# Performance work log

Hardware: AMD Instinct MI355X
Metric: run time of the kernel (lower is better)

The kernel has to match this reference:

```python
import jax, jax.numpy as jnp
import numpy as np

E, H, L = 512, 1024, 4
VS, VT = 32000, 32000
B, SS, TT = 64, 48, 48
PAD = 0


def _cell(x, h, c, Wih, Whh, bih, bhh):
    # torch.nn.LSTMCell math: gate order i, f, g, o
    g = x @ Wih.T + h @ Whh.T + bih + bhh
    i, f, gg, o = jnp.split(g, 4, axis=-1)
    c = jax.nn.sigmoid(f) * c + jax.nn.sigmoid(i) * jnp.tanh(gg)
    h = jax.nn.sigmoid(o) * jnp.tanh(c)
    return h, c


def setup_inputs() -> dict:
    key = jax.random.key(0)
    ks = jax.random.split(key, 14)
    s = 0.05
    d = {}
    d['src_tokens'] = jax.random.randint(ks[0], (SS, B), 0, VS, dtype=jnp.int32)
    d['tgt_tokens'] = jax.random.randint(ks[1], (TT, B), 0, VT, dtype=jnp.int32)
    d['src_emb'] = jax.random.normal(ks[2], (VS, E)) * s
    d['tgt_emb'] = jax.random.normal(ks[3], (VT, E)) * s
    d['enc_Wih0'] = jax.random.normal(ks[4], (4 * H, E)) * s
    d['enc_WihR'] = jax.random.normal(ks[5], (L - 1, 4 * H, H)) * s
    d['enc_Whh'] = jax.random.normal(ks[6], (L, 4 * H, H)) * s
    d['enc_bih'] = jnp.zeros((L, 4 * H))
    d['enc_bhh'] = jnp.zeros((L, 4 * H))
    d['dec_Wih0'] = jax.random.normal(ks[7], (4 * H, E + H)) * s
    d['dec_WihR'] = jax.random.normal(ks[8], (L - 1, 4 * H, H)) * s
    d['dec_Whh'] = jax.random.normal(ks[9], (L, 4 * H, H)) * s
    d['dec_bih'] = jnp.zeros((L, 4 * H))
    d['dec_bhh'] = jnp.zeros((L, 4 * H))
    d['att_vec_W'] = jax.random.normal(ks[10], (H, 2 * H)) * s
    d['readout_W'] = jax.random.normal(ks[11], (VT, H)) * s
    return d


def _forward(src_tokens, tgt_tokens, src_emb, tgt_emb, enc_Wih0, enc_WihR,
             enc_Whh, enc_bih, enc_bhh, dec_Wih0, dec_WihR, dec_Whh, dec_bih,
             dec_bhh, att_vec_W, readout_W):
    src_x = src_emb[src_tokens]                      # [SS, B, E]
    h0 = jnp.zeros((L, B, H), src_emb.dtype)
    c0 = jnp.zeros((L, B, H), src_emb.dtype)

    def enc_step(carry, x_t):
        h, c = carry
        inp = x_t
        hs, cs = [], []
        for l in range(L):
            Wih = enc_Wih0 if l == 0 else enc_WihR[l - 1]
            hn, cn = _cell(inp, h[l], c[l], Wih, enc_Whh[l], enc_bih[l], enc_bhh[l])
            hs.append(hn); cs.append(cn)
            inp = hn
        return (jnp.stack(hs), jnp.stack(cs)), inp

    (hT, cT), enc_out = jax.lax.scan(enc_step, (h0, c0), src_x)
    src_enc = enc_out.transpose(1, 0, 2)             # [B, SS, H]

    # decoder init: last encoder layer (h, c) copied to every decoder layer
    hd = jnp.tile(hT[-1][None], (L, 1, 1))
    cd = jnp.tile(cT[-1][None], (L, 1, 1))
    tgt_x = tgt_emb[tgt_tokens[:-1]]                 # [TT-1, B, E]
    att0 = jnp.zeros((B, H), src_emb.dtype)

    def dec_step(carry, y_t):
        h, c, att = carry
        inp = jnp.concatenate([y_t, att], axis=-1)   # input feeding
        hs, cs = [], []
        for l in range(L):
            Wih = dec_Wih0 if l == 0 else dec_WihR[l - 1]
            hn, cn = _cell(inp, h[l], c[l], Wih, dec_Whh[l], dec_bih[l], dec_bhh[l])
            hs.append(hn); cs.append(cn)
            inp = hn
        h_top = hs[-1]
        # global attention, 'dot' score (full-length seqs -> all-zero mask is a no-op)
        scores = jnp.einsum('bsh,bh->bs', src_enc, h_top)
        alpha = jax.nn.softmax(scores, axis=-1)
        ctx = jnp.einsum('bs,bsh->bh', alpha, src_enc)
        att_t = jnp.tanh(jnp.concatenate([h_top, ctx], axis=-1) @ att_vec_W.T)
        return (jnp.stack(hs), jnp.stack(cs), att_t), att_t

    _, att_ves = jax.lax.scan(dec_step, (hd, cd, att0), tgt_x)  # [TT-1, B, H]

    logp = jax.nn.log_softmax(att_ves @ readout_W.T, axis=-1)   # [TT-1, B, VT]
    gold = tgt_tokens[1:]
    gold_lp = jnp.take_along_axis(logp, gold[..., None], axis=-1)[..., 0]
    mask = (gold != PAD).astype(logp.dtype)
    return (gold_lp * mask).sum(axis=0)              # [B]


def reference(src_tokens, tgt_tokens, src_emb, tgt_emb, enc_Wih0, enc_WihR,
              enc_Whh, enc_bih, enc_bhh, dec_Wih0, dec_WihR, dec_Whh, dec_bih,
              dec_bhh, att_vec_W, readout_W):
    return _forward(src_tokens, tgt_tokens, src_emb, tgt_emb, enc_Wih0,
                    enc_WihR, enc_Whh, enc_bih, enc_bhh, dec_Wih0, dec_WihR,
                    dec_Whh, dec_bih, dec_bhh, att_vec_W, readout_W)
```

## Files before the change

### kernel.cpp

```cpp
#include <hip/hip_runtime.h>


typedef __attribute__((ext_vector_type(8))) short bf16x8;
typedef __attribute__((ext_vector_type(4))) float f32x4;

#define SMEM_BYTES 32768
#define SMEM_RO    49152

#define NMT_SYNC_LIGHT()                                   \
  do {                                                     \
    asm volatile("s_waitcnt lgkmcnt(0)" ::: "memory");     \
    __builtin_amdgcn_s_barrier();                          \
    __builtin_amdgcn_sched_barrier(0);                     \
  } while (0)

__device__ __forceinline__ float bf2f(ushort u) {
  union { uint i; float f; } v; v.i = ((uint)u) << 16; return v.f;
}
__device__ __forceinline__ ushort f2bf(float x) {
  union { float f; uint i; } v; v.f = x;
  uint r = (v.i + 0x7fffu + ((v.i >> 16) & 1u)) >> 16;
  return (ushort)r;
}
__device__ __forceinline__ float sigm(float x) {
  return __fdividef(1.f, 1.f + __expf(-x));
}
__device__ __forceinline__ float tanhf_fast(float x) {
  const float e = __expf(2.f * x);
  return 1.f - __fdividef(2.f, e + 1.f);
}

__device__ __forceinline__ void gemm_term(
    const ushort* __restrict__ A, int lda,
    const ushort* __restrict__ W, int ldw,
    int K, int m0, int n0,
    f32x4 acc[4], char* s)
{
  char* sA0 = s;
  char* sB0 = s + 8192;
  char* sA1 = s + 16384;
  char* sB1 = s + 24576;
  const int tid = threadIdx.x;
  const int lane = tid & 63;
  const int w = tid >> 6;
  const int r0 = tid >> 3;
  const int cge = (tid & 7) << 3;
  const ushort* Arow0 = A + (size_t)(m0 + r0) * lda + cge;
  const ushort* Arow1 = A + (size_t)(m0 + r0 + 32) * lda + cge;
  const ushort* Wrow0 = W + (size_t)(n0 + r0) * ldw + cge;
  const ushort* Wrow1 = W + (size_t)(n0 + r0 + 32) * ldw + cge;
  const int so0 = r0 * 128 + (((tid & 7) << 4) ^ ((r0 & 7) << 4));
  const int so1 = so0 + 4096;

  uint4 a0 = *reinterpret_cast<const uint4*>(Arow0);
  uint4 a1 = *reinterpret_cast<const uint4*>(Arow1);
  uint4 b0 = *reinterpret_cast<const uint4*>(Wrow0);
  uint4 b1 = *reinterpret_cast<const uint4*>(Wrow1);
  *reinterpret_cast<uint4*>(sA0 + so0) = a0;
  *reinterpret_cast<uint4*>(sA0 + so1) = a1;
  *reinterpret_cast<uint4*>(sB0 + so0) = b0;
  *reinterpret_cast<uint4*>(sB0 + so1) = b1;
  if (K > 64) {
    a0 = *reinterpret_cast<const uint4*>(Arow0 + 64);
    a1 = *reinterpret_cast<const uint4*>(Arow1 + 64);
    b0 = *reinterpret_cast<const uint4*>(Wrow0 + 64);
    b1 = *reinterpret_cast<const uint4*>(Wrow1 + 64);
  }
  const int axor = (lane & 7) << 4;
  const int arow = (w * 16 + (lane & 15)) * 128;
  const int brow = (lane & 15) * 128;
  const int kb0 = (lane >> 4) << 4;
  for (int kt = 0; kt < K; kt += 64) {
    char* cA = (kt & 64) ? sA1 : sA0;
    char* cB = (kt & 64) ? sB1 : sB0;
    char* nA = (kt & 64) ? sA0 : sA1;
    char* nB = (kt & 64) ? sB0 : sB1;
    __syncthreads();
    if (kt + 64 < K) {
      *reinterpret_cast<uint4*>(nA + so0) = a0;
      *reinterpret_cast<uint4*>(nA + so1) = a1;
      *reinterpret_cast<uint4*>(nB + so0) = b0;
      *reinterpret_cast<uint4*>(nB + so1) = b1;
      if (kt + 128 < K) {
        a0 = *reinterpret_cast<const uint4*>(Arow0 + kt + 128);
        a1 = *reinterpret_cast<const uint4*>(Arow1 + kt + 128);
        b0 = *reinterpret_cast<const uint4*>(Wrow0 + kt + 128);
        b1 = *reinterpret_cast<const uint4*>(Wrow1 + kt + 128);
      }
    }
#pragma unroll
    for (int ks = 0; ks < 2; ++ks) {
      const int kb = ks * 64 + kb0;
      bf16x8 af = *reinterpret_cast<const bf16x8*>(cA + arow + (kb ^ axor));
#pragma unroll
      for (int nf = 0; nf < 4; ++nf) {
        bf16x8 bfr = *reinterpret_cast<const bf16x8*>(
            cB + nf * 2048 + brow + (kb ^ axor));
        acc[nf] = __builtin_amdgcn_mfma_f32_16x16x32_bf16(af, bfr, acc[nf], 0, 0, 0);
      }
    }
  }
  __syncthreads();
}

__device__ __forceinline__ void store_f32(
    float* __restrict__ out, int ldo, int m0, int n0, f32x4 acc[4])
{
  const int tid = threadIdx.x, lane = tid & 63, w = tid >> 6;
  const int rbase = w * 16 + ((lane >> 4) << 2);
  const int cb = lane & 15;
#pragma unroll
  for (int nf = 0; nf < 4; ++nf)
#pragma unroll
    for (int r = 0; r < 4; ++r)
      out[(size_t)(m0 + rbase + r) * ldo + n0 + nf * 16 + cb] = acc[nf][r];
}

__device__ __forceinline__ void cell_store(
    float* smemF, f32x4 acc[4],
    float* __restrict__ c, ushort* __restrict__ hout,
    ushort* __restrict__ senc_t, int j0)
{
  const int tid = threadIdx.x, lane = tid & 63, w = tid >> 6;
  const int rbase = w * 16 + ((lane >> 4) << 2);
  const int cb = lane & 15;
  __syncthreads();
#pragma unroll
  for (int nf = 0; nf < 4; ++nf)
#pragma unroll
    for (int r = 0; r < 4; ++r)
      smemF[(rbase + r) * 68 + nf * 16 + cb] = acc[nf][r];
  __syncthreads();
#pragma unroll
  for (int i = 0; i < 4; ++i) {
    const int id = tid + i * 256;
    const int b = id >> 4, u = id & 15;
    const float g0 = smemF[b * 68 + u * 4 + 0];
    const float g1 = smemF[b * 68 + u * 4 + 1];
    const float g2 = smemF[b * 68 + u * 4 + 2];
    const float g3 = smemF[b * 68 + u * 4 + 3];
    const int off = b * 1024 + j0 + u;
    const float cold = c[off];
    const float cn = sigm(g1) * cold + sigm(g0) * tanhf_fast(g2);
    const float hv = sigm(g3) * tanhf_fast(cn);
    c[off] = cn;
    const ushort hb = f2bf(hv);
    hout[off] = hb;
    if (senc_t) senc_t[(size_t)b * 49152 + j0 + u] = hb;
  }
}

__global__ __launch_bounds__(256) void nmt_init(float* c, ushort* henc, ushort* attbf)
{
  const int idx = blockIdx.x * 256 + threadIdx.x;
  if (idx < 262144) c[idx] = 0.f;
  if (idx < 65536) {
    attbf[idx] = 0;
    henc[idx] = 0;
    henc[(size_t)1 * 49 * 65536 + idx] = 0;
    henc[(size_t)2 * 49 * 65536 + idx] = 0;
    henc[(size_t)3 * 49 * 65536 + idx] = 0;
  }
}

__global__ __launch_bounds__(256) void nmt_convperm(
    const float* __restrict__ in, ushort* __restrict__ out,
    int L, int Kin, int col0, int Kout)
{
  const size_t idx = (size_t)blockIdx.x * 256 + threadIdx.x;
  const size_t total = (size_t)L * 4096 * Kout;
  if (idx >= total) return;
  const int k = (int)(idx % Kout);
  const size_t rem = idx / Kout;
  const int rp = (int)(rem % 4096);
  const int l = (int)(rem / 4096);
  const int j = rp >> 2, g = rp & 3;
  out[idx] = f2bf(in[((size_t)l * 4096 + g * 1024 + j) * Kin + col0 + k]);
}

__global__ __launch_bounds__(256) void nmt_convplain(
    const float* __restrict__ in, ushort* __restrict__ out, size_t n)
{
  const size_t idx = (size_t)blockIdx.x * 256 + threadIdx.x;
  if (idx < n) out[idx] = f2bf(in[idx]);
}

__global__ __launch_bounds__(256) void nmt_bias(
    const float* __restrict__ bih, const float* __restrict__ bhh, float* __restrict__ bc)
{
  const int idx = blockIdx.x * 256 + threadIdx.x;
  if (idx >= 4 * 4096) return;
  const int rp = idx & 4095, l = idx >> 12;
  const int j = rp >> 2, g = rp & 3;
  bc[idx] = bih[l * 4096 + g * 1024 + j] + bhh[l * 4096 + g * 1024 + j];
}

__global__ __launch_bounds__(256) void nmt_gather(
    const int* __restrict__ tok, const float* __restrict__ emb,
    ushort* __restrict__ out, int rows)
{
  const size_t idx = (size_t)blockIdx.x * 256 + threadIdx.x;
  if (idx >= (size_t)rows * 512) return;
  const int k = (int)(idx & 511);
  const int r = (int)(idx >> 9);
  out[idx] = f2bf(emb[(size_t)tok[r] * 512 + k]);
}

__global__ __launch_bounds__(256) void nmt_pre(
    const ushort* __restrict__ A, const ushort* __restrict__ Wp,
    const float* __restrict__ bc0, float* __restrict__ out, int K)
{
  __shared__ __align__(16) char smem[SMEM_BYTES];
  const int m0 = blockIdx.x * 64, n0 = blockIdx.y * 64;
  const int lane = threadIdx.x & 63;
  const int cb = lane & 15;
  f32x4 acc[4];
#pragma unroll
  for (int nf = 0; nf < 4; ++nf) {
    const float bv = bc0[n0 + nf * 16 + cb];
#pragma unroll
    for (int r = 0; r < 4; ++r) acc[nf][r] = bv;
  }
  gemm_term(A, K, Wp, K, K, m0, n0, acc, smem);
  store_f32(out, 4096, m0, n0, acc);
}

__global__ __launch_bounds__(256) void nmt_decinit(
    const ushort* __restrict__ henc, float* c, ushort* h)
{
  const int idx = blockIdx.x * 256 + threadIdx.x;
  if (idx >= 65536) return;
  const ushort hv = henc[((size_t)3 * 49 + 48) * 65536 + idx];
  const float cv = c[3 * 65536 + idx];
  c[idx] = cv; c[65536 + idx] = cv; c[2 * 65536 + idx] = cv;
  h[idx] = hv; h[65536 + idx] = hv; h[2 * 65536 + idx] = hv; h[3 * 65536 + idx] = hv;
}

__global__ __launch_bounds__(256) void nmt_sv(
    const ushort* __restrict__ senc, const ushort* __restrict__ attW,
    ushort* __restrict__ SV)
{
  __shared__ __align__(16) char smem[SMEM_BYTES];
  const int b = blockIdx.x;
  const int n0 = blockIdx.y * 64;
  const int tid = threadIdx.x, lane = tid & 63, w = tid >> 6;
  const int rbase = w * 16 + ((lane >> 4) << 2), cb = lane & 15;
  f32x4 acc[4];
#pragma unroll
  for (int nf = 0; nf < 4; ++nf)
#pragma unroll
    for (int r = 0; r < 4; ++r) acc[nf][r] = 0.f;
  gemm_term(senc + (size_t)b * 49152, 1024, attW + 1024, 2048, 1024, 0, n0,
            acc, smem);
#pragma unroll
  for (int nf = 0; nf < 4; ++nf)
#pragma unroll
    for (int r = 0; r < 4; ++r) {
      const int row = rbase + r;
      if (row < 48)
        SV[(size_t)b * 49152 + row * 1024 + n0 + nf * 16 + cb] = f2bf(acc[nf][r]);
    }
}

__global__ __launch_bounds__(256) void nmt_enc_cell(
    int u, int lo, ushort* __restrict__ henc, ushort* __restrict__ srcenc,
    float* __restrict__ c,
    const ushort* __restrict__ WihR, const ushort* __restrict__ Whh,
    const float* __restrict__ X0, const float* __restrict__ bcE)
{
  __shared__ __align__(16) char smem[SMEM_BYTES];
  const int l = lo + blockIdx.y;
  const int t = u - l;
  const int n0 = blockIdx.x * 64;
  const int tid = threadIdx.x, lane = tid & 63, w = tid >> 6;
  const int rbase = w * 16 + ((lane >> 4) << 2), cb = lane & 15;
  f32x4 acc[4];
  if (l == 0) {
#pragma unroll
    for (int nf = 0; nf < 4; ++nf)
#pragma unroll
      for (int r = 0; r < 4; ++r)
        acc[nf][r] = X0[(size_t)t * 262144 + (size_t)(rbase + r) * 4096 + n0 + nf * 16 + cb];
  } else {
#pragma unroll
    for (int nf = 0; nf < 4; ++nf) {
      const float bv = bcE[l * 4096 + n0 + nf * 16 + cb];
#pragma unroll
      for (int r = 0; r < 4; ++r) acc[nf][r] = bv;
    }
    gemm_term(henc + ((size_t)(l - 1) * 49 + t + 1) * 65536, 1024,
              WihR + (size_t)(l - 1) * 4194304, 1024, 1024, 0, n0, acc, smem);
  }
  gemm_term(henc + ((size_t)l * 49 + t) * 65536, 1024,
            Whh + (size_t)l * 4194304, 1024, 1024, 0, n0, acc, smem);
  cell_store((float*)smem, acc, c + l * 65536,
             henc + ((size_t)l * 49 + t + 1) * 65536,
             (l == 3) ? (srcenc + t * 1024) : (ushort*)nullptr, n0 >> 2);
}

__global__ __launch_bounds__(256) void nmt_dec_stage(
    int l, const ushort* __restrict__ hp, ushort* __restrict__ hn,
    float* __restrict__ c,
    const ushort* __restrict__ Whh, const ushort* __restrict__ WihR,
    const ushort* __restrict__ Wd0a, const ushort* __restrict__ attbf,
    const float* __restrict__ Y0t, const float* __restrict__ bcD,
    float* __restrict__ pbuf)
{
  __shared__ __align__(16) char smem[SMEM_BYTES];
  const int n0 = blockIdx.x * 64;
  const int tid = threadIdx.x, lane = tid & 63, w = tid >> 6;
  const int rbase = w * 16 + ((lane >> 4) << 2), cb = lane & 15;
  f32x4 acc[4];
  if (blockIdx.y == 0) {
    if (l == 0) {
#pragma unroll
      for (int nf = 0; nf < 4; ++nf)
#pragma unroll
        for (int r = 0; r < 4; ++r) {
          const size_t o = (size_t)(rbase + r) * 4096 + n0 + nf * 16 + cb;
          acc[nf][r] = Y0t[o] + pbuf[o];
        }
      gemm_term(attbf, 1024, Wd0a, 1024, 1024, 0, n0, acc, smem);
    } else {
#pragma unroll
      for (int nf = 0; nf < 4; ++nf)
#pragma unroll
        for (int r = 0; r < 4; ++r)
          acc[nf][r] = pbuf[(size_t)l * 262144 + (size_t)(rbase + r) * 4096 + n0 + nf * 16 + cb];
      gemm_term(hn + (l - 1) * 65536, 1024, WihR + (size_t)(l - 1) * 4194304,
                1024, 1024, 0, n0, acc, smem);
    }
    cell_store((float*)smem, acc, c + l * 65536, hn + l * 65536,
               (ushort*)nullptr, n0 >> 2);
  } else {
    const int lp = (l + 1) & 3;
    if (lp == 0) {
#pragma unroll
      for (int nf = 0; nf < 4; ++nf)
#pragma unroll
        for (int r = 0; r < 4; ++r) acc[nf][r] = 0.f;
      gemm_term(hn, 1024, Whh, 1024, 1024, 0, n0, acc, smem);
    } else {
#pragma unroll
      for (int nf = 0; nf < 4; ++nf) {
        const float bv = bcD[lp * 4096 + n0 + nf * 16 + cb];
#pragma unroll
        for (int r = 0; r < 4; ++r) acc[nf][r] = bv;
      }
      gemm_term(hp + lp * 65536, 1024, Whh + (size_t)lp * 4194304,
                1024, 1024, 0, n0, acc, smem);
    }
    store_f32(pbuf + (size_t)lp * 262144, 4096, 0, n0, acc);
  }
}

__global__ __launch_bounds__(256) void nmt_partial0(
    const ushort* __restrict__ h0, const ushort* __restrict__ Whh0,
    float* __restrict__ pbuf)
{
  __shared__ __align__(16) char smem[SMEM_BYTES];
  const int n0 = blockIdx.x * 64;
  f32x4 acc[4];
#pragma unroll
  for (int nf = 0; nf < 4; ++nf)
#pragma unroll
    for (int r = 0; r < 4; ++r) acc[nf][r] = 0.f;
  gemm_term(h0, 1024, Whh0, 1024, 1024, 0, n0, acc, smem);
  store_f32(pbuf, 4096, 0, n0, acc);
}

__global__ __launch_bounds__(256) void nmt_attnAB(
    const ushort* __restrict__ h3, const ushort* __restrict__ senc,
    const ushort* __restrict__ SV, const ushort* __restrict__ attW,
    float* __restrict__ ctx2, float* __restrict__ hb)
{
  __shared__ __align__(16) char smem[SMEM_BYTES];
  const int bid = blockIdx.x;
  const int tid = threadIdx.x, lane = tid & 63, w = tid >> 6;
  if (bid < 64) {
    float* sc = (float*)smem;
    float* al = (float*)smem + 64;
    const int b = bid;
    const ushort* sb = senc + (size_t)b * 49152;
    const ushort* vb = SV + (size_t)b * 49152;
    float hreg[16];
#pragma unroll
    for (int q = 0; q < 16; ++q) hreg[q] = bf2f(h3[b * 1024 + lane * 16 + q]);
    for (int s = w; s < 48; s += 4) {
      const ushort* vr = sb + s * 1024 + lane * 16;
      float p = 0.f;
#pragma unroll
      for (int q = 0; q < 16; ++q) p += bf2f(vr[q]) * hreg[q];
      for (int d = 1; d < 64; d <<= 1) p += __shfl_xor(p, d);
      if (lane == 0) sc[s] = p;
    }
    __syncthreads();
    if (tid < 64) {
      const float v = (lane < 48) ? sc[lane] : -3.4e38f;
      float m = v;
      for (int d = 1; d < 64; d <<= 1) m = fmaxf(m, __shfl_xor(m, d));
      float e = (lane < 48) ? expf(v - m) : 0.f;
      float s = e;
      for (int d = 1; d < 64; d <<= 1) s += __shfl_xor(s, d);
      al[lane] = e / s;
    }
    __syncthreads();
    const int k0 = tid * 4;
    float a0 = 0, a1 = 0, a2 = 0, a3 = 0;
    for (int s = 0; s < 48; ++s) {
      const float als = al[s];
      const ushort* vr = vb + s * 1024 + k0;
      a0 += als * bf2f(vr[0]); a1 += als * bf2f(vr[1]);
      a2 += als * bf2f(vr[2]); a3 += als * bf2f(vr[3]);
    }
    ctx2[b * 1024 + k0 + 0] = a0; ctx2[b * 1024 + k0 + 1] = a1;
    ctx2[b * 1024 + k0 + 2] = a2; ctx2[b * 1024 + k0 + 3] = a3;
  } else {
    const int n0 = (bid - 64) * 64;
    f32x4 acc[4];
#pragma unroll
    for (int nf = 0; nf < 4; ++nf)
#pragma unroll
      for (int r = 0; r < 4; ++r) acc[nf][r] = 0.f;
    gemm_term(h3, 1024, attW, 2048, 1024, 0, n0, acc, smem);
    store_f32(hb, 1024, 0, n0, acc);
  }
}

__global__ __launch_bounds__(256) void nmt_attnSB(
    const float* __restrict__ ctx2, const float* __restrict__ hb,
    ushort* __restrict__ attbf, ushort* __restrict__ av_t)
{
  const int base = blockIdx.x * 1024 + threadIdx.x * 4;
#pragma unroll
  for (int k = 0; k < 4; ++k) {
    const int i = base + k;
    const ushort us = f2bf(tanhf_fast(hb[i] + ctx2[i]));
    attbf[i] = us;
    av_t[i] = us;
  }
}

__global__ __launch_bounds__(256) void nmt_readout(
    const ushort* __restrict__ attves, const ushort* __restrict__ routW,
    const int* __restrict__ tgt, float* __restrict__ pmax,
    float* __restrict__ psum, float* __restrict__ goldl)
{
  __shared__ __align__(16) char smem[SMEM_RO];
  const int g = blockIdx.x;
  const int n0 = blockIdx.y * 64;
  const int tid = threadIdx.x, lane = tid & 63, w = tid >> 6;
  const int rbase = w * 16 + ((lane >> 4) << 2), cb = lane & 15;
  const int r0 = tid >> 3;
  const int cge = (tid & 7) << 3;
  const int soX = r0 * 128 + (((tid & 7) << 4) ^ ((r0 & 7) << 4));
  const int axor = (lane & 7) << 4;
  const int arow = (w * 16 + (lane & 15)) * 128;
  const int brow = (lane & 15) * 128;
  const int kb0 = (lane >> 4) << 4;

  const ushort* A0r0 = attves + (size_t)(g * 128 + r0) * 1024 + cge;
  const ushort* A0r1 = attves + (size_t)(g * 128 + r0 + 32) * 1024 + cge;
  const ushort* A1r0 = attves + (size_t)(g * 128 + 64 + r0) * 1024 + cge;
  const ushort* A1r1 = attves + (size_t)(g * 128 + 64 + r0 + 32) * 1024 + cge;
  const ushort* Br0  = routW + (size_t)(n0 + r0) * 1024 + cge;
  const ushort* Br1  = routW + (size_t)(n0 + r0 + 32) * 1024 + cge;

  f32x4 acc[2][4];
#pragma unroll
  for (int mi = 0; mi < 2; ++mi)
#pragma unroll
    for (int nf = 0; nf < 4; ++nf)
#pragma unroll
      for (int r = 0; r < 4; ++r) acc[mi][nf][r] = 0.f;

  uint4 ra0 = *(const uint4*)(A0r0);
  uint4 ra1 = *(const uint4*)(A0r1);
  uint4 ra2 = *(const uint4*)(A1r0);
  uint4 ra3 = *(const uint4*)(A1r1);
  uint4 rb0 = *(const uint4*)(Br0);
  uint4 rb1 = *(const uint4*)(Br1);
  {
    char* sl = smem;
    *(uint4*)(sl + soX) = ra0;          *(uint4*)(sl + 4096 + soX) = ra1;
    *(uint4*)(sl + 8192 + soX) = ra2;   *(uint4*)(sl + 12288 + soX) = ra3;
    *(uint4*)(sl + 16384 + soX) = rb0;  *(uint4*)(sl + 20480 + soX) = rb1;
  }
  ra0 = *(const uint4*)(A0r0 + 64);
  ra1 = *(const uint4*)(A0r1 + 64);
  ra2 = *(const uint4*)(A1r0 + 64);
  ra3 = *(const uint4*)(A1r1 + 64);
  rb0 = *(const uint4*)(Br0 + 64);
  rb1 = *(const uint4*)(Br1 + 64);

  for (int kt = 0; kt < 1024; kt += 64) {
    NMT_SYNC_LIGHT();
    if (kt + 64 < 1024) {
      char* sl = smem + ((((kt >> 6) + 1) & 1) ? 24576 : 0);
      *(uint4*)(sl + soX) = ra0;          *(uint4*)(sl + 4096 + soX) = ra1;
      *(uint4*)(sl + 8192 + soX) = ra2;   *(uint4*)(sl + 12288 + soX) = ra3;
      *(uint4*)(sl + 16384 + soX) = rb0;  *(uint4*)(sl + 20480 + soX) = rb1;
      if (kt + 128 < 1024) {
        ra0 = *(const uint4*)(A0r0 + kt + 128);
        ra1 = *(const uint4*)(A0r1 + kt + 128);
        ra2 = *(const uint4*)(A1r0 + kt + 128);
        ra3 = *(const uint4*)(A1r1 + kt + 128);
        rb0 = *(const uint4*)(Br0 + kt + 128);
        rb1 = *(const uint4*)(Br1 + kt + 128);
      }
    }
    char* cur = smem + (((kt >> 6) & 1) ? 24576 : 0);
#pragma unroll
    for (int ks = 0; ks < 2; ++ks) {
      const int kb = (ks << 6) + kb0;
      bf16x8 bf0 = *(const bf16x8*)(cur + 16384 + 0 * 2048 + brow + (kb ^ axor));
      bf16x8 bf1 = *(const bf16x8*)(cur + 16384 + 1 * 2048 + brow + (kb ^ axor));
      bf16x8 bf2 = *(const bf16x8*)(cur + 16384 + 2 * 2048 + brow + (kb ^ axor));
      bf16x8 bf3 = *(const bf16x8*)(cur + 16384 + 3 * 2048 + brow + (kb ^ axor));
      bf16x8 af0 = *(const bf16x8*)(cur + arow + (kb ^ axor));
      bf16x8 af1 = *(const bf16x8*)(cur + 8192 + arow + (kb ^ axor));
      acc[0][0] = __builtin_amdgcn_mfma_f32_16x16x32_bf16(af0, bf0, acc[0][0], 0, 0, 0);
      acc[0][1] = __builtin_amdgcn_mfma_f32_16x16x32_bf16(af0, bf1, acc[0][1], 0, 0, 0);
      acc[0][2] = __builtin_amdgcn_mfma_f32_16x16x32_bf16(af0, bf2, acc[0][2], 0, 0, 0);
      acc[0][3] = __builtin_amdgcn_mfma_f32_16x16x32_bf16(af0, bf3, acc[0][3], 0, 0, 0);
      acc[1][0] = __builtin_amdgcn_mfma_f32_16x16x32_bf16(af1, bf0, acc[1][0], 0, 0, 0);
      acc[1][1] = __builtin_amdgcn_mfma_f32_16x16x32_bf16(af1, bf1, acc[1][1], 0, 0, 0);
      acc[1][2] = __builtin_amdgcn_mfma_f32_16x16x32_bf16(af1, bf2, acc[1][2], 0, 0, 0);
      acc[1][3] = __builtin_amdgcn_mfma_f32_16x16x32_bf16(af1, bf3, acc[1][3], 0, 0, 0);
    }
  }

#pragma unroll
  for (int mi = 0; mi < 2; ++mi) {
    const int gm = g * 2 + mi;
    if (gm >= 47) continue;
#pragma unroll
    for (int r = 0; r < 4; ++r) {
      float lm = fmaxf(fmaxf(acc[mi][0][r], acc[mi][1][r]),
                       fmaxf(acc[mi][2][r], acc[mi][3][r]));
      for (int d = 1; d < 16; d <<= 1) lm = fmaxf(lm, __shfl_xor(lm, d));
      float ls = 0.f;
#pragma unroll
      for (int nf = 0; nf < 4; ++nf) ls += expf(acc[mi][nf][r] - lm);
      for (int d = 1; d < 16; d <<= 1) ls += __shfl_xor(ls, d);
      const int grow = gm * 64 + rbase + r;
      if (cb == 0) {
        pmax[(size_t)grow * 500 + blockIdx.y] = lm;
        psum[(size_t)grow * 500 + blockIdx.y] = ls;
      }
      const int t = grow >> 6, b = grow & 63;
      const int gold = tgt[(t + 1) * 64 + b];
#pragma unroll
      for (int nf = 0; nf < 4; ++nf)
        if (n0 + nf * 16 + cb == gold) goldl[grow] = acc[mi][nf][r];
    }
  }
}

__global__ __launch_bounds__(64) void nmt_combine(
    const float* __restrict__ pmax, const float* __restrict__ psum,
    const float* __restrict__ goldl, const int* __restrict__ tgt,
    float* __restrict__ lpm)
{
  const int row = blockIdx.x;
  const int lane = threadIdx.x;
  float m = -3.4e38f, s = 0.f;
  for (int i = lane; i < 500; i += 64) {
    const float pm = pmax[(size_t)row * 500 + i];
    const float ps = psum[(size_t)row * 500 + i];
    if (pm > m) { s = s * expf(m - pm) + ps; m = pm; }
    else        { s += ps * expf(pm - m); }
  }
  for (int d = 1; d < 64; d <<= 1) {
    const float om = __shfl_xor(m, d), os = __shfl_xor(s, d);
    if (om > m) { s = s * expf(m - om) + os; m = om; }
    else        { s += os * expf(om - m); }
  }
  if (lane == 0) {
    const int t = row >> 6, b = row & 63;
    const int gold = tgt[(t + 1) * 64 + b];
    const float lp = goldl[row] - m - logf(s);
    lpm[row] = (gold != 0) ? lp : 0.f;
  }
}

__global__ __launch_bounds__(64) void nmt_final(
    const float* __restrict__ lpm, float* __restrict__ out)
{
  const int b = threadIdx.x;
  float s = 0.f;
  for (int t = 0; t < 47; ++t) s += lpm[t * 64 + b];
  out[b] = s;
}

extern "C" void kernel_launch(void* const* d_in, const int* in_sizes, int n_in,
                              void* d_out, int out_size, void* d_ws, size_t ws_size,
                              hipStream_t stream)
{
  (void)in_sizes; (void)n_in; (void)out_size; (void)ws_size;
  const int*   src_tok  = (const int*)d_in[0];
  const int*   tgt_tok  = (const int*)d_in[1];
  const float* src_emb  = (const float*)d_in[2];
  const float* tgt_emb  = (const float*)d_in[3];
  const float* eWih0    = (const float*)d_in[4];
  const float* eWihR    = (const float*)d_in[5];
  const float* eWhh     = (const float*)d_in[6];
  const float* ebih     = (const float*)d_in[7];
  const float* ebhh     = (const float*)d_in[8];
  const float* dWih0    = (const float*)d_in[9];
  const float* dWihR    = (const float*)d_in[10];
  const float* dWhh     = (const float*)d_in[11];
  const float* dbih     = (const float*)d_in[12];
  const float* dbhh     = (const float*)d_in[13];
  const float* attW_f   = (const float*)d_in[14];
  const float* routW_f  = (const float*)d_in[15];

  char* p = (char*)d_ws;
  auto alloc = [&](size_t bytes) { void* r = (void*)p; p += (bytes + 255) & ~(size_t)255; return r; };
  ushort* eWih0p = (ushort*)alloc((size_t)4096 * 512 * 2);
  ushort* eWihRp = (ushort*)alloc((size_t)3 * 4096 * 1024 * 2);
  ushort* eWhhp  = (ushort*)alloc((size_t)4 * 4096 * 1024 * 2);
  ushort* dWih0y = (ushort*)alloc((size_t)4096 * 512 * 2);
  ushort* dWih0a = (ushort*)alloc((size_t)4096 * 1024 * 2);
  ushort* dWihRp = (ushort*)alloc((size_t)3 * 4096 * 1024 * 2);
  ushort* dWhhp  = (ushort*)alloc((size_t)4 * 4096 * 1024 * 2);
  ushort* attWb  = (ushort*)alloc((size_t)1024 * 2048 * 2);
  ushort* routWb = (ushort*)alloc((size_t)32000 * 1024 * 2);
  ushort* srcx   = (ushort*)alloc((size_t)3072 * 512 * 2);
  ushort* tgtx   = (ushort*)alloc((size_t)3008 * 512 * 2);
  ushort* henc   = (ushort*)alloc((size_t)4 * 49 * 65536 * 2);
  ushort* hA     = (ushort*)alloc((size_t)4 * 65536 * 2);
  ushort* hB     = (ushort*)alloc((size_t)4 * 65536 * 2);
  ushort* srcenc = (ushort*)alloc((size_t)64 * 49152 * 2);
  ushort* SVbuf  = (ushort*)alloc((size_t)64 * 49152 * 2);
  ushort* attbf  = (ushort*)alloc((size_t)65536 * 2);
  ushort* attves = (ushort*)alloc((size_t)3072 * 1024 * 2);
  float*  ctx2   = (float*)alloc((size_t)65536 * 4);
  float*  hbuf   = (float*)alloc((size_t)65536 * 4);
  float*  pbuf   = (float*)alloc((size_t)4 * 262144 * 4);
  float*  X0     = (float*)alloc((size_t)3072 * 4096 * 4);
  float*  Y0     = (float*)alloc((size_t)3008 * 4096 * 4);
  float*  bcE    = (float*)alloc((size_t)16384 * 4);
  float*  bcD    = (float*)alloc((size_t)16384 * 4);
  float*  cbuf   = (float*)alloc((size_t)4 * 65536 * 4);
  float*  pmaxb  = (float*)alloc((size_t)3008 * 500 * 4);
  float*  psumb  = (float*)alloc((size_t)3008 * 500 * 4);
  float*  goldl  = (float*)alloc((size_t)3008 * 4);
  float*  lpm    = (float*)alloc((size_t)3008 * 4);

  const dim3 B256(256);
  auto g1 = [](size_t n) { return dim3((unsigned)((n + 255) / 256)); };

  nmt_init<<<g1(262144), B256, 0, stream>>>(cbuf, henc, attbf);

  nmt_convperm<<<g1((size_t)4096 * 512), B256, 0, stream>>>(eWih0, eWih0p, 1, 512, 0, 512);
  nmt_convperm<<<g1((size_t)3 * 4096 * 1024), B256, 0, stream>>>(eWihR, eWihRp, 3, 1024, 0, 1024);
  nmt_convperm<<<g1((size_t)4 * 4096 * 1024), B256, 0, stream>>>(eWhh, eWhhp, 4, 1024, 0, 1024);
  nmt_convperm<<<g1((size_t)4096 * 512), B256, 0, stream>>>(dWih0, dWih0y, 1, 1536, 0, 512);
  nmt_convperm<<<g1((size_t)4096 * 1024), B256, 0, stream>>>(dWih0, dWih0a, 1, 1536, 512, 1024);
  nmt_convperm<<<g1((size_t)3 * 4096 * 1024), B256, 0, stream>>>(dWihR, dWihRp, 3, 1024, 0, 1024);
  nmt_convperm<<<g1((size_t)4 * 4096 * 1024), B256, 0, stream>>>(dWhh, dWhhp, 4, 1024, 0, 1024);
  nmt_convplain<<<g1((size_t)1024 * 2048), B256, 0, stream>>>(attW_f, attWb, (size_t)1024 * 2048);
  nmt_convplain<<<g1((size_t)32000 * 1024), B256, 0, stream>>>(routW_f, routWb, (size_t)32000 * 1024);
  nmt_bias<<<g1(16384), B256, 0, stream>>>(ebih, ebhh, bcE);
  nmt_bias<<<g1(16384), B256, 0, stream>>>(dbih, dbhh, bcD);
  nmt_gather<<<g1((size_t)3072 * 512), B256, 0, stream>>>(src_tok, src_emb, srcx, 3072);
  nmt_gather<<<g1((size_t)3008 * 512), B256, 0, stream>>>(tgt_tok, tgt_emb, tgtx, 3008);

  nmt_pre<<<dim3(48, 64), B256, 0, stream>>>(srcx, eWih0p, bcE, X0, 512);
  nmt_pre<<<dim3(47, 64), B256, 0, stream>>>(tgtx, dWih0y, bcD, Y0, 512);

  for (int u = 0; u < 51; ++u) {
    const int lo = (u > 47) ? (u - 47) : 0;
    const int hi = (u < 3) ? u : 3;
    nmt_enc_cell<<<dim3(64, hi - lo + 1), B256, 0, stream>>>(
        u, lo, henc, srcenc, cbuf, eWihRp, eWhhp, X0, bcE);
  }
  nmt_decinit<<<g1(65536), B256, 0, stream>>>(henc, cbuf, hA);
  nmt_sv<<<dim3(64, 16), B256, 0, stream>>>(srcenc, attWb, SVbuf);
  nmt_partial0<<<dim3(64), B256, 0, stream>>>(hA, dWhhp, pbuf);

  for (int t = 0; t < 47; ++t) {
    ushort* hp = (t & 1) ? hB : hA;
    ushort* hn = (t & 1) ? hA : hB;
    for (int l = 0; l < 4; ++l) {
      nmt_dec_stage<<<dim3(64, 2), B256, 0, stream>>>(
          l, hp, hn, cbuf, dWhhp, dWihRp, dWih0a, attbf,
          Y0 + (size_t)t * 262144, bcD, pbuf);
    }
    nmt_attnAB<<<dim3(80), B256, 0, stream>>>(hn + 3 * 65536, srcenc, SVbuf,
                                              attWb, ctx2, hbuf);
    nmt_attnSB<<<dim3(64), B256, 0, stream>>>(ctx2, hbuf, attbf,
                                              attves + (size_t)t * 65536);
  }

  nmt_readout<<<dim3(24, 500), B256, 0, stream>>>(attves, routWb, tgt_tok,
                                                  pmaxb, psumb, goldl);
  nmt_combine<<<dim3(3008), dim3(64), 0, stream>>>(pmaxb, psumb, goldl, tgt_tok, lpm);
  nmt_final<<<dim3(1), dim3(64), 0, stream>>>(lpm, (float*)d_out);
}
```

Baseline: 4.191 ms.

## Fuse attention tanh/bf16 pack into decoder layer-0 GEMM load and batch attves

Removes the per-step nmt_attnSB kernel by having the decoder layer-0 stage compute tanh(hb+ctx) on the fly while staging the A operand into shared memory. hb and ctx are kept per step in large fp32 buffers, and all attention vectors are converted to bf16 for the readout in one batched kernel after the loop. This saves 47 kernel launches and their serial dependency gaps. In exchange, the layer-0 GEMM reads fp32 operands and uses 64KB of shared memory, which may reduce occupancy, and the tanh is recomputed by each of the 64 column blocks.

```diff
diff --git a/kernel.cpp b/kernel.cpp
--- a/kernel.cpp
+++ b/kernel.cpp
@@ -5,6 +5,7 @@
 typedef __attribute__((ext_vector_type(4))) float f32x4;
 
 #define SMEM_BYTES 32768
+#define SMEM_A     65536
 #define SMEM_RO    49152
 
 #define NMT_SYNC_LIGHT()                                   \
@@ -21,6 +22,9 @@
   union { float f; uint i; } v; v.f = x;
   uint r = (v.i + 0x7fffu + ((v.i >> 16) & 1u)) >> 16;
   return (ushort)r;
+}
+__device__ __forceinline__ uint pack2(float x, float y) {
+  return (uint)f2bf(x) | ((uint)f2bf(y) << 16);
 }
 __device__ __forceinline__ float sigm(float x) {
   return __fdividef(1.f, 1.f + __expf(-x));
@@ -103,6 +107,119 @@
   __syncthreads();
 }
 
+__device__ __forceinline__ void att_loadf(
+    const float* H0, const float* H1, const float* C0, const float* C1,
+    int kt, float4* fh, float4* fc)
+{
+#pragma unroll
+  for (int q = 0; q < 8; ++q) {
+    const int rh = q >> 2, sub = (q >> 1) & 1, vq = q & 1;
+    const float* hp_ = rh ? H1 : H0;
+    const float* cp_ = rh ? C1 : C0;
+    fh[q] = *reinterpret_cast<const float4*>(hp_ + kt + sub * 64 + vq * 4);
+    fc[q] = *reinterpret_cast<const float4*>(cp_ + kt + sub * 64 + vq * 4);
+  }
+}
+
+__device__ __forceinline__ void att_store(
+    char* buf, int soX, const float4* fh, const float4* fc)
+{
+#pragma unroll
+  for (int rh = 0; rh < 2; ++rh)
+#pragma unroll
+    for (int sub = 0; sub < 2; ++sub) {
+      const int q0 = rh * 4 + sub * 2;
+      const float4 u = fh[q0], v = fc[q0];
+      const float4 u2 = fh[q0 + 1], v2 = fc[q0 + 1];
+      uint4 o;
+      o.x = pack2(tanhf_fast(u.x + v.x), tanhf_fast(u.y + v.y));
+      o.y = pack2(tanhf_fast(u.z + v.z), tanhf_fast(u.w + v.w));
+      o.z = pack2(tanhf_fast(u2.x + v2.x), tanhf_fast(u2.y + v2.y));
+      o.w = pack2(tanhf_fast(u2.z + v2.z), tanhf_fast(u2.w + v2.w));
+      *reinterpret_cast<uint4*>(buf + sub * 8192 + rh * 4096 + soX) = o;
+    }
+}
+
+__device__ __forceinline__ void gemm_att(
+    const float* __restrict__ H, const float* __restrict__ C2,
+    const ushort* __restrict__ W, int ldw, int n0,
+    f32x4 acc[4], char* s)
+{
+  char* sA0 = s;
+  char* sB0 = s + 16384;
+  char* sA1 = s + 32768;
+  char* sB1 = s + 49152;
+  const int tid = threadIdx.x;
+  const int lane = tid & 63;
+  const int w = tid >> 6;
+  const int r0 = tid >> 3;
+  const int cge = (tid & 7) << 3;
+  const int soX = r0 * 128 + (((tid & 7) << 4) ^ ((r0 & 7) << 4));
+  const ushort* Wr0 = W + (size_t)(n0 + r0) * ldw + cge;
+  const ushort* Wr1 = W + (size_t)(n0 + r0 + 32) * ldw + cge;
+  const float* H0 = H + r0 * 1024 + cge;
+  const float* H1 = H + (r0 + 32) * 1024 + cge;
+  const float* C0 = C2 + r0 * 1024 + cge;
+  const float* C1 = C2 + (r0 + 32) * 1024 + cge;
+
+  float4 fh[8], fc[8];
+  uint4 b0, b1, b2, b3;
+  att_loadf(H0, H1, C0, C1, 0, fh, fc);
+  att_store(sA0, soX, fh, fc);
+  b0 = *reinterpret_cast<const uint4*>(Wr0);
+  b1 = *reinterpret_cast<const uint4*>(Wr1);
+  b2 = *reinterpret_cast<const uint4*>(Wr0 + 64);
+  b3 = *reinterpret_cast<const uint4*>(Wr1 + 64);
+  *reinterpret_cast<uint4*>(sB0 + soX) = b0;
+  *reinterpret_cast<uint4*>(sB0 + 4096 + soX) = b1;
+  *reinterpret_cast<uint4*>(sB0 + 8192 + soX) = b2;
+  *reinterpret_cast<uint4*>(sB0 + 12288 + soX) = b3;
+  att_loadf(H0, H1, C0, C1, 128, fh, fc);
+  b0 = *reinterpret_cast<const uint4*>(Wr0 + 128);
+  b1 = *reinterpret_cast<const uint4*>(Wr1 + 128);
+  b2 = *reinterpret_cast<const uint4*>(Wr0 + 192);
+  b3 = *reinterpret_cast<const uint4*>(Wr1 + 192);
+
+  const int axor = (lane & 7) << 4;
+  const int arow = (w * 16 + (lane & 15)) * 128;
+  const int brow = (lane & 15) * 128;
+  const int kb0 = (lane >> 4) << 4;
+  for (int kt = 0; kt < 1024; kt += 128) {
+    char* cA = (kt & 128) ? sA1 : sA0;
+    char* cB = (kt & 128) ? sB1 : sB0;
+    char* nA = (kt & 128) ? sA0 : sA1;
+    char* nB = (kt & 128) ? sB0 : sB1;
+    NMT_SYNC_LIGHT();
+    if (kt + 128 < 1024) {
+      att_store(nA, soX, fh, fc);
+      *reinterpret_cast<uint4*>(nB + soX) = b0;
+      *reinterpret_cast<uint4*>(nB + 4096 + soX) = b1;
+      *reinterpret_cast<uint4*>(nB + 8192 + soX) = b2;
+      *reinterpret_cast<uint4*>(nB + 12288 + soX) = b3;
+      if (kt + 256 < 1024) {
+        att_loadf(H0, H1, C0, C1, kt + 256, fh, fc);
+        b0 = *reinterpret_cast<const uint4*>(Wr0 + kt + 256);
+        b1 = *reinterpret_cast<const uint4*>(Wr1 + kt + 256);
+        b2 = *reinterpret_cast<const uint4*>(Wr0 + kt + 320);
+        b3 = *reinterpret_cast<const uint4*>(Wr1 + kt + 320);
+      }
+    }
+#pragma unroll
+    for (int ks = 0; ks < 4; ++ks) {
+      const int sb = (ks >> 1) * 8192;
+      const int kb = ((ks & 1) << 6) + kb0;
+      bf16x8 af = *reinterpret_cast<const bf16x8*>(cA + sb + arow + (kb ^ axor));
+#pragma unroll
+      for (int nf = 0; nf < 4; ++nf) {
+        bf16x8 bfr = *reinterpret_cast<const bf16x8*>(
+            cB + sb + nf * 2048 + brow + (kb ^ axor));
+        acc[nf] = __builtin_amdgcn_mfma_f32_16x16x32_bf16(af, bfr, acc[nf], 0, 0, 0);
+      }
+    }
+  }
+  __syncthreads();
+}
+
 __device__ __forceinline__ void store_f32(
     float* __restrict__ out, int ldo, int m0, int n0, f32x4 acc[4])
 {
@@ -150,12 +267,14 @@
   }
 }
 
-__global__ __launch_bounds__(256) void nmt_init(float* c, ushort* henc, ushort* attbf)
+__global__ __launch_bounds__(256) void nmt_init(
+    float* c, ushort* henc, float* hbAll, float* ctxAll)
 {
   const int idx = blockIdx.x * 256 + threadIdx.x;
   if (idx < 262144) c[idx] = 0.f;
   if (idx < 65536) {
-    attbf[idx] = 0;
+    hbAll[idx] = 0.f;
+    ctxAll[idx] = 0.f;
     henc[idx] = 0;
     henc[(size_t)1 * 49 * 65536 + idx] = 0;
     henc[(size_t)2 * 49 * 65536 + idx] = 0;
@@ -302,11 +421,12 @@
     int l, const ushort* __restrict__ hp, ushort* __restrict__ hn,
     float* __restrict__ c,
     const ushort* __restrict__ Whh, const ushort* __restrict__ WihR,
-    const ushort* __restrict__ Wd0a, const ushort* __restrict__ attbf,
+    const ushort* __restrict__ Wd0a,
+    const float* __restrict__ hbprev, const float* __restrict__ ctxprev,
     const float* __restrict__ Y0t, const float* __restrict__ bcD,
     float* __restrict__ pbuf)
 {
-  __shared__ __align__(16) char smem[SMEM_BYTES];
+  __shared__ __align__(16) char smem[SMEM_A];
   const int n0 = blockIdx.x * 64;
   const int tid = threadIdx.x, lane = tid & 63, w = tid >> 6;
   const int rbase = w * 16 + ((lane >> 4) << 2), cb = lane & 15;
@@ -320,7 +440,7 @@
           const size_t o = (size_t)(rbase + r) * 4096 + n0 + nf * 16 + cb;
           acc[nf][r] = Y0t[o] + pbuf[o];
         }
-      gemm_term(attbf, 1024, Wd0a, 1024, 1024, 0, n0, acc, smem);
+      gemm_att(hbprev, ctxprev, Wd0a, 1024, n0, acc, smem);
     } else {
 #pragma unroll
       for (int nf = 0; nf < 4; ++nf)
@@ -427,17 +547,15 @@
   }
 }
 
-__global__ __launch_bounds__(256) void nmt_attnSB(
-    const float* __restrict__ ctx2, const float* __restrict__ hb,
-    ushort* __restrict__ attbf, ushort* __restrict__ av_t)
-{
-  const int base = blockIdx.x * 1024 + threadIdx.x * 4;
+__global__ __launch_bounds__(256) void nmt_attves_k(
+    const float* __restrict__ hbAll, const float* __restrict__ ctxAll,
+    ushort* __restrict__ attves)
+{
+  const int i = blockIdx.x * 1024 + threadIdx.x * 4;
 #pragma unroll
   for (int k = 0; k < 4; ++k) {
-    const int i = base + k;
-    const ushort us = f2bf(tanhf_fast(hb[i] + ctx2[i]));
-    attbf[i] = us;
-    av_t[i] = us;
+    const int j = i + k;
+    attves[j] = f2bf(tanhf_fast(hbAll[j + 65536] + ctxAll[j + 65536]));
   }
 }
 
@@ -633,10 +751,9 @@
   ushort* hB     = (ushort*)alloc((size_t)4 * 65536 * 2);
   ushort* srcenc = (ushort*)alloc((size_t)64 * 49152 * 2);
   ushort* SVbuf  = (ushort*)alloc((size_t)64 * 49152 * 2);
-  ushort* attbf  = (ushort*)alloc((size_t)65536 * 2);
   ushort* attves = (ushort*)alloc((size_t)3072 * 1024 * 2);
-  float*  ctx2   = (float*)alloc((size_t)65536 * 4);
-  float*  hbuf   = (float*)alloc((size_t)65536 * 4);
+  float*  hbAll  = (float*)alloc((size_t)48 * 65536 * 4);
+  float*  ctxAll = (float*)alloc((size_t)48 * 65536 * 4);
   float*  pbuf   = (float*)alloc((size_t)4 * 262144 * 4);
   float*  X0     = (float*)alloc((size_t)3072 * 4096 * 4);
   float*  Y0     = (float*)alloc((size_t)3008 * 4096 * 4);
@@ -651,7 +768,7 @@
   const dim3 B256(256);
   auto g1 = [](size_t n) { return dim3((unsigned)((n + 255) / 256)); };
 
-  nmt_init<<<g1(262144), B256, 0, stream>>>(cbuf, henc, attbf);
+  nmt_init<<<g1(262144), B256, 0, stream>>>(cbuf, henc, hbAll, ctxAll);
 
   nmt_convperm<<<g1((size_t)4096 * 512), B256, 0, stream>>>(eWih0, eWih0p, 1, 512, 0, 512);
   nmt_convperm<<<g1((size_t)3 * 4096 * 1024), B256, 0, stream>>>(eWihR, eWihRp, 3, 1024, 0, 1024);
@@ -685,14 +802,15 @@
     ushort* hn = (t & 1) ? hA : hB;
     for (int l = 0; l < 4; ++l) {
       nmt_dec_stage<<<dim3(64, 2), B256, 0, stream>>>(
-          l, hp, hn, cbuf, dWhhp, dWihRp, dWih0a, attbf,
+          l, hp, hn, cbuf, dWhhp, dWihRp, dWih0a,
+          hbAll + (size_t)t * 65536, ctxAll + (size_t)t * 65536,
           Y0 + (size_t)t * 262144, bcD, pbuf);
     }
-    nmt_attnAB<<<dim3(80), B256, 0, stream>>>(hn + 3 * 65536, srcenc, SVbuf,
-                                              attWb, ctx2, hbuf);
-    nmt_attnSB<<<dim3(64), B256, 0, stream>>>(ctx2, hbuf, attbf,
-                                              attves + (size_t)t * 65536);
-  }
+    nmt_attnAB<<<dim3(80), B256, 0, stream>>>(
+        hn + 3 * 65536, srcenc, SVbuf, attWb,
+        ctxAll + (size_t)(t + 1) * 65536, hbAll + (size_t)(t + 1) * 65536);
+  }
+  nmt_attves_k<<<dim3(3008), B256, 0, stream>>>(hbAll, ctxAll, attves);
 
   nmt_readout<<<dim3(24, 500), B256, 0, stream>>>(attves, routWb, tgt_tok,
                                                   pmaxb, psumb, goldl);
```

New measurement: 4.673 ms. +11.5%, slower.

## Split encoder cells into skewed input-projection and recurrent ticks

Applied to the files above, without the earlier changes.

The encoder wavefront is rescheduled with a skew of two ticks per layer. Each layer's input projection (WihR times the lower layer's h) now runs one tick ahead in separate partial blocks and is stored to a new fp32 buffer. Cell blocks then only do the recurrent Whh GEMM plus the gate math. This roughly halves the serial GEMM depth per launch, at the cost of three extra launches and extra fp32 traffic for the partial sums. One pbufE slot per layer is read by a cell block and rewritten by a partial block within the same launch, which is a potential cross-block race.

```diff
diff --git a/kernel.cpp b/kernel.cpp
--- a/kernel.cpp
+++ b/kernel.cpp
@@ -262,40 +262,53 @@
     }
 }
 
-__global__ __launch_bounds__(256) void nmt_enc_cell(
-    int u, int lo, ushort* __restrict__ henc, ushort* __restrict__ srcenc,
+__global__ __launch_bounds__(256) void nmt_enc_tick(
+    int v, int lc0, int ncell, int lp0,
+    ushort* __restrict__ henc, ushort* __restrict__ srcenc,
     float* __restrict__ c,
     const ushort* __restrict__ WihR, const ushort* __restrict__ Whh,
-    const float* __restrict__ X0, const float* __restrict__ bcE)
+    const float* __restrict__ X0, const float* __restrict__ bcE,
+    float* __restrict__ pbufE)
 {
   __shared__ __align__(16) char smem[SMEM_BYTES];
-  const int l = lo + blockIdx.y;
-  const int t = u - l;
   const int n0 = blockIdx.x * 64;
   const int tid = threadIdx.x, lane = tid & 63, w = tid >> 6;
   const int rbase = w * 16 + ((lane >> 4) << 2), cb = lane & 15;
   f32x4 acc[4];
-  if (l == 0) {
-#pragma unroll
-    for (int nf = 0; nf < 4; ++nf)
-#pragma unroll
-      for (int r = 0; r < 4; ++r)
-        acc[nf][r] = X0[(size_t)t * 262144 + (size_t)(rbase + r) * 4096 + n0 + nf * 16 + cb];
+  if ((int)blockIdx.y < ncell) {
+    const int l = lc0 + blockIdx.y;
+    const int t = v - 2 * l;
+    if (l == 0) {
+#pragma unroll
+      for (int nf = 0; nf < 4; ++nf)
+#pragma unroll
+        for (int r = 0; r < 4; ++r)
+          acc[nf][r] = X0[(size_t)t * 262144 + (size_t)(rbase + r) * 4096 + n0 + nf * 16 + cb];
+    } else {
+#pragma unroll
+      for (int nf = 0; nf < 4; ++nf)
+#pragma unroll
+        for (int r = 0; r < 4; ++r)
+          acc[nf][r] = pbufE[(size_t)l * 262144 + (size_t)(rbase + r) * 4096 + n0 + nf * 16 + cb];
+    }
+    gemm_term(henc + ((size_t)l * 49 + t) * 65536, 1024,
+              Whh + (size_t)l * 4194304, 1024, 1024, 0, n0, acc, smem);
+    cell_store((float*)smem, acc, c + l * 65536,
+               henc + ((size_t)l * 49 + t + 1) * 65536,
+               (l == 3) ? (srcenc + t * 1024) : (ushort*)nullptr, n0 >> 2);
   } else {
+    const int l = lp0 + (blockIdx.y - ncell);
+    const int tp = v + 1 - 2 * l;
 #pragma unroll
     for (int nf = 0; nf < 4; ++nf) {
       const float bv = bcE[l * 4096 + n0 + nf * 16 + cb];
 #pragma unroll
       for (int r = 0; r < 4; ++r) acc[nf][r] = bv;
     }
-    gemm_term(henc + ((size_t)(l - 1) * 49 + t + 1) * 65536, 1024,
+    gemm_term(henc + ((size_t)(l - 1) * 49 + tp + 1) * 65536, 1024,
               WihR + (size_t)(l - 1) * 4194304, 1024, 1024, 0, n0, acc, smem);
-  }
-  gemm_term(henc + ((size_t)l * 49 + t) * 65536, 1024,
-            Whh + (size_t)l * 4194304, 1024, 1024, 0, n0, acc, smem);
-  cell_store((float*)smem, acc, c + l * 65536,
-             henc + ((size_t)l * 49 + t + 1) * 65536,
-             (l == 3) ? (srcenc + t * 1024) : (ushort*)nullptr, n0 >> 2);
+    store_f32(pbufE + (size_t)l * 262144, 4096, 0, n0, acc);
+  }
 }
 
 __global__ __launch_bounds__(256) void nmt_dec_stage(
@@ -638,6 +651,7 @@
   float*  ctx2   = (float*)alloc((size_t)65536 * 4);
   float*  hbuf   = (float*)alloc((size_t)65536 * 4);
   float*  pbuf   = (float*)alloc((size_t)4 * 262144 * 4);
+  float*  pbufE  = (float*)alloc((size_t)4 * 262144 * 4);
   float*  X0     = (float*)alloc((size_t)3072 * 4096 * 4);
   float*  Y0     = (float*)alloc((size_t)3008 * 4096 * 4);
   float*  bcE    = (float*)alloc((size_t)16384 * 4);
@@ -670,11 +684,16 @@
   nmt_pre<<<dim3(48, 64), B256, 0, stream>>>(srcx, eWih0p, bcE, X0, 512);
   nmt_pre<<<dim3(47, 64), B256, 0, stream>>>(tgtx, dWih0y, bcD, Y0, 512);
 
-  for (int u = 0; u < 51; ++u) {
-    const int lo = (u > 47) ? (u - 47) : 0;
-    const int hi = (u < 3) ? u : 3;
-    nmt_enc_cell<<<dim3(64, hi - lo + 1), B256, 0, stream>>>(
-        u, lo, henc, srcenc, cbuf, eWihRp, eWhhp, X0, bcE);
+  for (int v = 0; v < 54; ++v) {
+    int lc0 = (v > 47) ? ((v - 47 + 1) / 2) : 0;
+    int lc1 = (v / 2 < 3) ? (v / 2) : 3;
+    int ncell = lc1 - lc0 + 1;
+    int lp0 = (v + 1 > 47) ? ((v + 1 - 47 + 1) / 2) : 1;
+    if (lp0 < 1) lp0 = 1;
+    int lp1 = ((v + 1) / 2 < 3) ? ((v + 1) / 2) : 3;
+    int npart = (lp1 >= lp0) ? (lp1 - lp0 + 1) : 0;
+    nmt_enc_tick<<<dim3(64, ncell + npart), B256, 0, stream>>>(
+        v, lc0, ncell, lp0, henc, srcenc, cbuf, eWihRp, eWhhp, X0, bcE, pbufE);
   }
   nmt_decinit<<<g1(65536), B256, 0, stream>>>(henc, cbuf, hA);
   nmt_sv<<<dim3(64, 16), B256, 0, stream>>>(srcenc, attWb, SVbuf);
```

Measured after the change: 3.993 ms. 1.05x faster.
